# Performance work log

Measured on AMD Instinct MI355X. Metric: run time of the kernel, lower is better.

## Reference

```python
import jax, jax.numpy as jnp
import numpy as np

B, S, D = 2, 2048, 2048
H, DH = 16, 128  # heads, dhead


def setup_inputs() -> dict:
    key = jax.random.key(0)
    k1, k2, k3 = jax.random.split(key, 3)
    x = jax.random.normal(k1, (B, S, D), dtype=jnp.float32)
    # torch Linear weights: [out_features, in_features], fan_in-scaled init
    w_in = jax.random.normal(k2, (3 * H * DH, D), dtype=jnp.float32) * (1.0 / np.sqrt(D))
    w_out = jax.random.normal(k3, (D, H * DH), dtype=jnp.float32) * (1.0 / np.sqrt(H * DH))
    return {"x": x, "w_in": w_in, "w_out": w_out}


def reference(x, w_in, w_out):
    b, s, _ = x.shape
    # input projection (no bias): [b, s, 3*H*DH]
    projected = jnp.einsum("bsd,ed->bse", x, w_in)
    # view(b, s, H, 3*DH) then chunk along last dim -> q, k, v each [b, s, H, DH]
    projected = projected.reshape(b, s, H, 3 * DH)
    q, k, v = jnp.split(projected, 3, axis=-1)
    # naive path: scores [b, H, s, s]
    scores = jnp.einsum("bqhd,bkhd->bhqk", q, k) * (1.0 / np.sqrt(DH))
    # causal mask (tril keeps, upper triangle -> -inf)
    causal_mask = jnp.tril(jnp.ones((s, s), dtype=bool))
    scores = jnp.where(causal_mask, scores, jnp.float32(-jnp.inf))
    attn = jax.nn.softmax(scores, axis=-1)
    # PV: [b, s, H, DH]
    out = jnp.einsum("bhqk,bkhd->bqhd", attn, v)
    out = out.reshape(b, s, H * DH)
    # output projection (no bias): [b, s, D]
    return jnp.einsum("bse,de->bsd", out, w_out)
```

## Files before the change

kernel.cpp:

```cpp
#include <hip/hip_runtime.h>
#include <hip/hip_bf16.h>
#include <math.h>


typedef short bf16x8 __attribute__((ext_vector_type(8)));
typedef float f32x4 __attribute__((ext_vector_type(4)));

#define NEG_BIG -30000.0f

__device__ __forceinline__ short f2bf(float f) {
    union { float f; unsigned u; } v; v.f = f;
    unsigned r = v.u + 0x7fffu + ((v.u >> 16) & 1u);
    return (short)(r >> 16);
}

__device__ __forceinline__ int pack2bf(float a, float b) {
    return (int)((((unsigned)f2bf(b)) << 16) | (((unsigned)f2bf(a)) & 0xffffu));
}

#define GLDS16(g, l) \
    __builtin_amdgcn_global_load_lds((const __attribute__((address_space(1))) void*)(g), \
                                     (__attribute__((address_space(3))) void*)(l), 16, 0, 0)

__global__ __launch_bounds__(256) void cvt_f32_bf16(const float* __restrict__ src,
                                                    short* __restrict__ dst, int n) {
    int i = (blockIdx.x * blockDim.x + threadIdx.x) * 4;
    if (i < n) {
        float4 v = *(const float4*)(src + i);
        short4 o;
        o.x = f2bf(v.x); o.y = f2bf(v.y); o.z = f2bf(v.z); o.w = f2bf(v.w);
        *(short4*)(dst + i) = o;
    }
}

template <int BN, bool F32OUT>
__global__ __launch_bounds__(256) void gemm_bt(const short* __restrict__ A,
                                               const short* __restrict__ Bm,
                                               void* __restrict__ Cv,
                                               int N, int K) {
    constexpr int NT = BN / 32;
    constexpr int SUBA = 128 * 32;
    constexpr int SUBB = BN * 32;
    __shared__ short sA[2 * SUBA];
    __shared__ short sB[2 * SUBB];
    const int lane = threadIdx.x & 63;
    const int w = threadIdx.x >> 6;
    const int l15 = lane & 15, quad = lane >> 4;
    const int bm0 = blockIdx.y * 128, bn0 = blockIdx.x * BN;

    const int c1 = w * 64 + lane;
    const short* gA = A + (size_t)(bm0 + (c1 >> 2)) * K + (c1 & 3) * 8;
    const short* gB = Bm + (size_t)(bn0 + (c1 >> 2)) * K + (c1 & 3) * 8;
    const size_t half64 = (size_t)64 * K;
    short* lA1 = sA + w * 512;
    short* lA2 = sA + 2048 + w * 512;
    short* lB1 = sB + w * 512;
    short* lB2 = sB + 2048 + w * 512;

    const int wm = (w >> 1) * 64, wn = (w & 1) * (BN / 2);
    const short* pa = sA + (wm + l15) * 32 + quad * 8;
    const short* pb = sB + (wn + l15) * 32 + quad * 8;

    f32x4 acc[4][NT] = {};
    for (int k0 = 0; k0 < K; k0 += 64) {
        #pragma unroll
        for (int s = 0; s < 2; s++) {
            const int ks = k0 + s * 32;
            GLDS16(gA + ks, lA1 + s * SUBA);
            GLDS16(gA + half64 + ks, lA2 + s * SUBA);
            GLDS16(gB + ks, lB1 + s * SUBB);
            if constexpr (BN == 128) GLDS16(gB + half64 + ks, lB2 + s * SUBB);
        }
        __syncthreads();
        #pragma unroll
        for (int s = 0; s < 2; s++) {
            bf16x8 af[4], bf[NT];
            #pragma unroll
            for (int mt = 0; mt < 4; mt++) af[mt] = *(const bf16x8*)(pa + s * SUBA + mt * 512);
            #pragma unroll
            for (int nt = 0; nt < NT; nt++) bf[nt] = *(const bf16x8*)(pb + s * SUBB + nt * 512);
            #pragma unroll
            for (int mt = 0; mt < 4; mt++)
                #pragma unroll
                for (int nt = 0; nt < NT; nt++)
                    acc[mt][nt] = __builtin_amdgcn_mfma_f32_16x16x32_bf16(af[mt], bf[nt], acc[mt][nt], 0, 0, 0);
        }
        __syncthreads();
    }
    #pragma unroll
    for (int mt = 0; mt < 4; mt++)
        #pragma unroll
        for (int nt = 0; nt < NT; nt++)
            #pragma unroll
            for (int r = 0; r < 4; r++) {
                int row = bm0 + wm + mt * 16 + quad * 4 + r;
                int col = bn0 + wn + nt * 16 + l15;
                if (F32OUT)
                    ((float*)Cv)[(size_t)row * N + col] = acc[mt][nt][r];
                else
                    ((short*)Cv)[(size_t)row * N + col] = f2bf(acc[mt][nt][r]);
            }
}

#define VP 40
__global__ __launch_bounds__(512) void attn_kernel(const short* __restrict__ P,
                                                   short* __restrict__ O) {
    constexpr int S = 2048, ROWW = 6144, HD = 2048;
    const int id = blockIdx.x;
    const int b = id >> 8;
    const int rr = id & 255;
    const int h = rr & 15;
    const int t0 = rr >> 4;
    const int qt = b ? (15 - t0) : t0;
    const int wave = threadIdx.x >> 6, lane = threadIdx.x & 63;
    const int l15 = lane & 15, quad = lane >> 4;
    const int qRow = qt * 128 + wave * 16;
    const short* Pb = P + (size_t)b * S * ROWW;
    const short* Qp = Pb + h * 384;
    const short* Kp = Qp + 128;
    const short* Vp = Qp + 256;

    __shared__ short sK[2][32 * 128];
    __shared__ short sVt[2][128 * VP];

    bf16x8 qf[4];
    #pragma unroll
    for (int f = 0; f < 4; f++)
        qf[f] = *(const bf16x8*)(Qp + (size_t)(qRow + l15) * ROWW + f * 32 + quad * 8);

    const bool isK = wave < 4;
    const int c1 = (wave & 3) * 64 + lane;
    const int krow1 = c1 >> 4;
    const int kcol = ((c1 & 15) ^ (krow1 & 15)) * 8;
    const short* gK1 = Kp + (size_t)krow1 * ROWW + kcol;
    const short* gK2 = Kp + (size_t)(krow1 + 16) * ROWW + kcol;
    const int ldsOff1 = (wave & 3) * 512;
    const int ldsOff2 = 2048 + (wave & 3) * 512;
    const int vt = (int)threadIdx.x - 256;
    const int vKey = vt & 31;
    const int vD0 = (vt >> 5) * 8;
    const short* gV = Vp + (size_t)vKey * ROWW + vD0;

    const int kTiles = qt * 4 + 4;
    const float scale = 0.08838834764831845f;
    const int qG = qRow + l15;

    f32x4 accO[8] = {};
    float m_i = NEG_BIG, l_i = 0.f;

    if (isK) {
        GLDS16(gK1, &sK[0][ldsOff1]);
        GLDS16(gK2, &sK[0][ldsOff2]);
    } else {
        bf16x8 v0 = *(const bf16x8*)(gV);
        bf16x8 v1 = *(const bf16x8*)(gV + 64);
        #pragma unroll
        for (int j = 0; j < 8; j++) {
            sVt[0][(vD0 + j) * VP + vKey] = v0[j];
            sVt[0][(vD0 + 64 + j) * VP + vKey] = v1[j];
        }
    }
    __syncthreads();

    for (int kt = 0; kt < kTiles; kt++) {
        const int cur = kt & 1, nxt = cur ^ 1;
        const bool pre = (kt + 1 < kTiles);
        bf16x8 v0n, v1n;
        if (pre) {
            const size_t kOff = (size_t)(kt + 1) * 32 * ROWW;
            if (isK) {
                GLDS16(gK1 + kOff, &sK[nxt][ldsOff1]);
                GLDS16(gK2 + kOff, &sK[nxt][ldsOff2]);
            } else {
                v0n = *(const bf16x8*)(gV + kOff);
                v1n = *(const bf16x8*)(gV + kOff + 64);
            }
        }
        f32x4 sc[2] = {};
        #pragma unroll
        for (int hh = 0; hh < 2; hh++) {
            const int row = hh * 16 + l15;
            #pragma unroll
            for (int f = 0; f < 4; f++) {
                const int jj = (4 * f + quad) ^ l15;
                bf16x8 kf = *(const bf16x8*)(&sK[cur][row * 128 + jj * 8]);
                sc[hh] = __builtin_amdgcn_mfma_f32_16x16x32_bf16(kf, qf[f], sc[hh], 0, 0, 0);
            }
        }
        #pragma unroll
        for (int hh = 0; hh < 2; hh++)
            #pragma unroll
            for (int r = 0; r < 4; r++) {
                int key = kt * 32 + hh * 16 + quad * 4 + r;
                float v = sc[hh][r] * scale;
                sc[hh][r] = (key <= qG) ? v : NEG_BIG;
            }
        float mloc = sc[0][0];
        #pragma unroll
        for (int r = 1; r < 4; r++) mloc = fmaxf(mloc, sc[0][r]);
        #pragma unroll
        for (int r = 0; r < 4; r++) mloc = fmaxf(mloc, sc[1][r]);
        mloc = fmaxf(mloc, __shfl_xor(mloc, 16));
        mloc = fmaxf(mloc, __shfl_xor(mloc, 32));
        const float nm = fmaxf(m_i, mloc);
        const float alpha = __expf(m_i - nm);
        m_i = nm;
        float ssum = 0.f;
        #pragma unroll
        for (int hh = 0; hh < 2; hh++)
            #pragma unroll
            for (int r = 0; r < 4; r++) {
                float p = __expf(sc[hh][r] - nm);
                sc[hh][r] = p;
                ssum += p;
            }
        ssum += __shfl_xor(ssum, 16);
        ssum += __shfl_xor(ssum, 32);
        l_i = alpha * l_i + ssum;
        #pragma unroll
        for (int t = 0; t < 8; t++)
            #pragma unroll
            for (int r = 0; r < 4; r++) accO[t][r] *= alpha;
        const int d00 = pack2bf(sc[0][0], sc[0][1]);
        const int d01 = pack2bf(sc[0][2], sc[0][3]);
        const int d10 = pack2bf(sc[1][0], sc[1][1]);
        const int d11 = pack2bf(sc[1][2], sc[1][3]);
        const int srcA = l15 + ((quad & 1) << 5);
        const int srcB = srcA + 16;
        const int s00 = __shfl(d00, srcA), s01 = __shfl(d01, srcA);
        const int s02 = __shfl(d00, srcB), s03 = __shfl(d01, srcB);
        const int s10 = __shfl(d10, srcA), s11 = __shfl(d11, srcA);
        const int s12 = __shfl(d10, srcB), s13 = __shfl(d11, srcB);
        union { int i[4]; bf16x8 v; } pu;
        const bool lo = quad < 2;
        pu.i[0] = lo ? s00 : s10;
        pu.i[1] = lo ? s01 : s11;
        pu.i[2] = lo ? s02 : s12;
        pu.i[3] = lo ? s03 : s13;
        const bf16x8 pf = pu.v;
        #pragma unroll
        for (int t = 0; t < 8; t++) {
            bf16x8 vf = *(const bf16x8*)(&sVt[cur][(t * 16 + l15) * VP + quad * 8]);
            accO[t] = __builtin_amdgcn_mfma_f32_16x16x32_bf16(vf, pf, accO[t], 0, 0, 0);
        }
        if (pre && !isK) {
            #pragma unroll
            for (int j = 0; j < 8; j++) {
                sVt[nxt][(vD0 + j) * VP + vKey] = v0n[j];
                sVt[nxt][(vD0 + 64 + j) * VP + vKey] = v1n[j];
            }
        }
        __syncthreads();
    }
    const float inv = 1.0f / l_i;
    #pragma unroll
    for (int t = 0; t < 8; t++) {
        short4 st;
        st.x = f2bf(accO[t][0] * inv);
        st.y = f2bf(accO[t][1] * inv);
        st.z = f2bf(accO[t][2] * inv);
        st.w = f2bf(accO[t][3] * inv);
        *(short4*)(&O[(size_t)(b * S + qG) * HD + h * 128 + t * 16 + quad * 4]) = st;
    }
}

extern "C" void kernel_launch(void* const* d_in, const int* in_sizes, int n_in,
                              void* d_out, int out_size, void* d_ws, size_t ws_size,
                              hipStream_t stream) {
    const float* x     = (const float*)d_in[0];
    const float* w_in  = (const float*)d_in[1];
    const float* w_out = (const float*)d_in[2];
    float* out = (float*)d_out;

    short* Pbuf   = (short*)d_ws;
    short* xObuf  = Pbuf  + (size_t)4096 * 6144;
    short* winb   = xObuf + (size_t)8388608;
    short* woutb  = winb  + (size_t)6144 * 2048;

    dim3 blk(256, 1, 1);
    const int nx = 2 * 2048 * 2048, nwi = 6144 * 2048, nwo = 2048 * 2048;
    hipLaunchKernelGGL(cvt_f32_bf16, dim3(nx / 1024), blk, 0, stream, x, xObuf, nx);
    hipLaunchKernelGGL(cvt_f32_bf16, dim3(nwi / 1024), blk, 0, stream, w_in, winb, nwi);
    hipLaunchKernelGGL(cvt_f32_bf16, dim3(nwo / 1024), blk, 0, stream, w_out, woutb, nwo);
    hipLaunchKernelGGL((gemm_bt<128, false>), dim3(48, 32, 1), blk, 0, stream, xObuf, winb, (void*)Pbuf, 6144, 2048);
    hipLaunchKernelGGL(attn_kernel, dim3(512, 1, 1), dim3(512, 1, 1), 0, stream, Pbuf, xObuf);
    hipLaunchKernelGGL((gemm_bt<128, true>), dim3(16, 32, 1), blk, 0, stream, xObuf, woutb, (void*)out, 2048, 2048);
}
```

Baseline: 387.3 us.

## Use 64-key attention tiles, skip fully masked tiles, and lazily rescale softmax

Doubles the key tile from 32 to 64 rows per iteration, halving the number of loop iterations and barriers while doubling LDS buffers for K and transposed V. Each wave now skips score and PV work for tiles lying entirely above its causal diagonal. The online softmax only rescales the accumulator and row sum when the running max grows by more than a threshold of 8, which avoids many exp and multiply passes. This trades more LDS and registers per block, and slightly different numerics from the lazy max update, for less per-tile overhead.

```diff
diff --git a/kernel.cpp b/kernel.cpp
--- a/kernel.cpp
+++ b/kernel.cpp
@@ -102,7 +102,7 @@
             }
 }
 
-#define VP 40
+#define VP2 72
 __global__ __launch_bounds__(512) void attn_kernel(const short* __restrict__ P,
                                                    short* __restrict__ O) {
     constexpr int S = 2048, ROWW = 6144, HD = 2048;
@@ -120,8 +120,8 @@
     const short* Kp = Qp + 128;
     const short* Vp = Qp + 256;
 
-    __shared__ short sK[2][32 * 128];
-    __shared__ short sVt[2][128 * VP];
+    __shared__ short sK[2][64 * 128];
+    __shared__ short sVt[2][128 * VP2];
 
     bf16x8 qf[4];
     #pragma unroll
@@ -134,14 +134,19 @@
     const int kcol = ((c1 & 15) ^ (krow1 & 15)) * 8;
     const short* gK1 = Kp + (size_t)krow1 * ROWW + kcol;
     const short* gK2 = Kp + (size_t)(krow1 + 16) * ROWW + kcol;
+    const short* gK3 = Kp + (size_t)(krow1 + 32) * ROWW + kcol;
+    const short* gK4 = Kp + (size_t)(krow1 + 48) * ROWW + kcol;
     const int ldsOff1 = (wave & 3) * 512;
-    const int ldsOff2 = 2048 + (wave & 3) * 512;
+    const int ldsOff2 = 2048 + ldsOff1;
+    const int ldsOff3 = 4096 + ldsOff1;
+    const int ldsOff4 = 6144 + ldsOff1;
     const int vt = (int)threadIdx.x - 256;
     const int vKey = vt & 31;
     const int vD0 = (vt >> 5) * 8;
     const short* gV = Vp + (size_t)vKey * ROWW + vD0;
-
-    const int kTiles = qt * 4 + 4;
+    const short* gV2 = Vp + (size_t)(vKey + 32) * ROWW + vD0;
+
+    const int kTiles = qt * 2 + 2;
     const float scale = 0.08838834764831845f;
     const int qG = qRow + l15;
 
@@ -151,13 +156,19 @@
     if (isK) {
         GLDS16(gK1, &sK[0][ldsOff1]);
         GLDS16(gK2, &sK[0][ldsOff2]);
+        GLDS16(gK3, &sK[0][ldsOff3]);
+        GLDS16(gK4, &sK[0][ldsOff4]);
     } else {
         bf16x8 v0 = *(const bf16x8*)(gV);
         bf16x8 v1 = *(const bf16x8*)(gV + 64);
+        bf16x8 v2 = *(const bf16x8*)(gV2);
+        bf16x8 v3 = *(const bf16x8*)(gV2 + 64);
         #pragma unroll
         for (int j = 0; j < 8; j++) {
-            sVt[0][(vD0 + j) * VP + vKey] = v0[j];
-            sVt[0][(vD0 + 64 + j) * VP + vKey] = v1[j];
+            sVt[0][(vD0 + j) * VP2 + vKey] = v0[j];
+            sVt[0][(vD0 + 64 + j) * VP2 + vKey] = v1[j];
+            sVt[0][(vD0 + j) * VP2 + vKey + 32] = v2[j];
+            sVt[0][(vD0 + 64 + j) * VP2 + vKey + 32] = v3[j];
         }
     }
     __syncthreads();
@@ -165,89 +176,102 @@
     for (int kt = 0; kt < kTiles; kt++) {
         const int cur = kt & 1, nxt = cur ^ 1;
         const bool pre = (kt + 1 < kTiles);
-        bf16x8 v0n, v1n;
+        bf16x8 v0n, v1n, v2n, v3n;
         if (pre) {
-            const size_t kOff = (size_t)(kt + 1) * 32 * ROWW;
+            const size_t kOff = (size_t)(kt + 1) * 64 * ROWW;
             if (isK) {
                 GLDS16(gK1 + kOff, &sK[nxt][ldsOff1]);
                 GLDS16(gK2 + kOff, &sK[nxt][ldsOff2]);
+                GLDS16(gK3 + kOff, &sK[nxt][ldsOff3]);
+                GLDS16(gK4 + kOff, &sK[nxt][ldsOff4]);
             } else {
                 v0n = *(const bf16x8*)(gV + kOff);
                 v1n = *(const bf16x8*)(gV + kOff + 64);
-            }
-        }
-        f32x4 sc[2] = {};
-        #pragma unroll
-        for (int hh = 0; hh < 2; hh++) {
-            const int row = hh * 16 + l15;
+                v2n = *(const bf16x8*)(gV2 + kOff);
+                v3n = *(const bf16x8*)(gV2 + kOff + 64);
+            }
+        }
+        if (kt * 64 <= qRow + 15) {
+            f32x4 sc[4] = {};
             #pragma unroll
             for (int f = 0; f < 4; f++) {
-                const int jj = (4 * f + quad) ^ l15;
-                bf16x8 kf = *(const bf16x8*)(&sK[cur][row * 128 + jj * 8]);
-                sc[hh] = __builtin_amdgcn_mfma_f32_16x16x32_bf16(kf, qf[f], sc[hh], 0, 0, 0);
-            }
-        }
-        #pragma unroll
-        for (int hh = 0; hh < 2; hh++)
-            #pragma unroll
-            for (int r = 0; r < 4; r++) {
-                int key = kt * 32 + hh * 16 + quad * 4 + r;
-                float v = sc[hh][r] * scale;
-                sc[hh][r] = (key <= qG) ? v : NEG_BIG;
-            }
-        float mloc = sc[0][0];
-        #pragma unroll
-        for (int r = 1; r < 4; r++) mloc = fmaxf(mloc, sc[0][r]);
-        #pragma unroll
-        for (int r = 0; r < 4; r++) mloc = fmaxf(mloc, sc[1][r]);
-        mloc = fmaxf(mloc, __shfl_xor(mloc, 16));
-        mloc = fmaxf(mloc, __shfl_xor(mloc, 32));
-        const float nm = fmaxf(m_i, mloc);
-        const float alpha = __expf(m_i - nm);
-        m_i = nm;
-        float ssum = 0.f;
-        #pragma unroll
-        for (int hh = 0; hh < 2; hh++)
-            #pragma unroll
-            for (int r = 0; r < 4; r++) {
-                float p = __expf(sc[hh][r] - nm);
-                sc[hh][r] = p;
-                ssum += p;
-            }
-        ssum += __shfl_xor(ssum, 16);
-        ssum += __shfl_xor(ssum, 32);
-        l_i = alpha * l_i + ssum;
-        #pragma unroll
-        for (int t = 0; t < 8; t++)
-            #pragma unroll
-            for (int r = 0; r < 4; r++) accO[t][r] *= alpha;
-        const int d00 = pack2bf(sc[0][0], sc[0][1]);
-        const int d01 = pack2bf(sc[0][2], sc[0][3]);
-        const int d10 = pack2bf(sc[1][0], sc[1][1]);
-        const int d11 = pack2bf(sc[1][2], sc[1][3]);
-        const int srcA = l15 + ((quad & 1) << 5);
-        const int srcB = srcA + 16;
-        const int s00 = __shfl(d00, srcA), s01 = __shfl(d01, srcA);
-        const int s02 = __shfl(d00, srcB), s03 = __shfl(d01, srcB);
-        const int s10 = __shfl(d10, srcA), s11 = __shfl(d11, srcA);
-        const int s12 = __shfl(d10, srcB), s13 = __shfl(d11, srcB);
-        union { int i[4]; bf16x8 v; } pu;
-        const bool lo = quad < 2;
-        pu.i[0] = lo ? s00 : s10;
-        pu.i[1] = lo ? s01 : s11;
-        pu.i[2] = lo ? s02 : s12;
-        pu.i[3] = lo ? s03 : s13;
-        const bf16x8 pf = pu.v;
-        #pragma unroll
-        for (int t = 0; t < 8; t++) {
-            bf16x8 vf = *(const bf16x8*)(&sVt[cur][(t * 16 + l15) * VP + quad * 8]);
-            accO[t] = __builtin_amdgcn_mfma_f32_16x16x32_bf16(vf, pf, accO[t], 0, 0, 0);
+                const int jj = ((4 * f + quad) ^ l15) * 8;
+                #pragma unroll
+                for (int hh = 0; hh < 4; hh++) {
+                    bf16x8 kf = *(const bf16x8*)(&sK[cur][(hh * 16 + l15) * 128 + jj]);
+                    sc[hh] = __builtin_amdgcn_mfma_f32_16x16x32_bf16(kf, qf[f], sc[hh], 0, 0, 0);
+                }
+            }
+            #pragma unroll
+            for (int hh = 0; hh < 4; hh++)
+                #pragma unroll
+                for (int r = 0; r < 4; r++) {
+                    int key = kt * 64 + hh * 16 + quad * 4 + r;
+                    float v = sc[hh][r] * scale;
+                    sc[hh][r] = (key <= qG) ? v : NEG_BIG;
+                }
+            float mloc = sc[0][0];
+            #pragma unroll
+            for (int hh = 0; hh < 4; hh++)
+                #pragma unroll
+                for (int r = 0; r < 4; r++) mloc = fmaxf(mloc, sc[hh][r]);
+            mloc = fmaxf(mloc, __shfl_xor(mloc, 16));
+            mloc = fmaxf(mloc, __shfl_xor(mloc, 32));
+            if (!__all(mloc <= m_i + 8.0f)) {
+                const float nm = fmaxf(m_i, mloc);
+                const float alpha = __expf(m_i - nm);
+                m_i = nm;
+                l_i *= alpha;
+                #pragma unroll
+                for (int t = 0; t < 8; t++)
+                    #pragma unroll
+                    for (int r = 0; r < 4; r++) accO[t][r] *= alpha;
+            }
+            float ssum = 0.f;
+            #pragma unroll
+            for (int hh = 0; hh < 4; hh++)
+                #pragma unroll
+                for (int r = 0; r < 4; r++) {
+                    float p = __expf(sc[hh][r] - m_i);
+                    sc[hh][r] = p;
+                    ssum += p;
+                }
+            ssum += __shfl_xor(ssum, 16);
+            ssum += __shfl_xor(ssum, 32);
+            l_i += ssum;
+            #pragma unroll
+            for (int s = 0; s < 2; s++) {
+                const int d00 = pack2bf(sc[2 * s][0], sc[2 * s][1]);
+                const int d01 = pack2bf(sc[2 * s][2], sc[2 * s][3]);
+                const int d10 = pack2bf(sc[2 * s + 1][0], sc[2 * s + 1][1]);
+                const int d11 = pack2bf(sc[2 * s + 1][2], sc[2 * s + 1][3]);
+                const int srcA = l15 + ((quad & 1) << 5);
+                const int srcB = srcA + 16;
+                const int s00 = __shfl(d00, srcA), s01 = __shfl(d01, srcA);
+                const int s02 = __shfl(d00, srcB), s03 = __shfl(d01, srcB);
+                const int s10 = __shfl(d10, srcA), s11 = __shfl(d11, srcA);
+                const int s12 = __shfl(d10, srcB), s13 = __shfl(d11, srcB);
+                union { int i[4]; bf16x8 v; } pu;
+                const bool lo = quad < 2;
+                pu.i[0] = lo ? s00 : s10;
+                pu.i[1] = lo ? s01 : s11;
+                pu.i[2] = lo ? s02 : s12;
+                pu.i[3] = lo ? s03 : s13;
+                const bf16x8 pf = pu.v;
+                #pragma unroll
+                for (int t = 0; t < 8; t++) {
+                    bf16x8 vf = *(const bf16x8*)(&sVt[cur][(t * 16 + l15) * VP2 + s * 32 + quad * 8]);
+                    accO[t] = __builtin_amdgcn_mfma_f32_16x16x32_bf16(vf, pf, accO[t], 0, 0, 0);
+                }
+            }
         }
         if (pre && !isK) {
             #pragma unroll
             for (int j = 0; j < 8; j++) {
-                sVt[nxt][(vD0 + j) * VP + vKey] = v0n[j];
-                sVt[nxt][(vD0 + 64 + j) * VP + vKey] = v1n[j];
+                sVt[nxt][(vD0 + j) * VP2 + vKey] = v0n[j];
+                sVt[nxt][(vD0 + 64 + j) * VP2 + vKey] = v1n[j];
+                sVt[nxt][(vD0 + j) * VP2 + vKey + 32] = v2n[j];
+                sVt[nxt][(vD0 + 64 + j) * VP2 + vKey + 32] = v3n[j];
             }
         }
         __syncthreads();
```

Result: no change. 394.6 us (+1.9%).
